# Optimization experiments

Measured on AMD Instinct MI355X. Metric: run time of the kernel, lower is better.

Reference implementation:

```python
import jax, jax.numpy as jnp
import numpy as np
import math

N_HEAD = 16
K_SPARSE = 64

def setup_inputs() -> dict:
    key = jax.random.key(0)
    ks = jax.random.split(key, 12)
    B, T, C = 1, 2048, 1024
    s = 0.02
    return {
        "x":   jax.random.normal(ks[0], (B, T, C), jnp.float32),
        "Wq":  jax.random.normal(ks[1], (C, C), jnp.float32) * s,
        "bq":  jax.random.normal(ks[2], (C,), jnp.float32) * s,
        "Wk":  jax.random.normal(ks[3], (C, C), jnp.float32) * s,
        "bk":  jax.random.normal(ks[4], (C,), jnp.float32) * s,
        "Wv":  jax.random.normal(ks[5], (C, C), jnp.float32) * s,
        "bv":  jax.random.normal(ks[6], (C,), jnp.float32) * s,
        "Wo":  jax.random.normal(ks[7], (C, C), jnp.float32) * s,
        "bo":  jax.random.normal(ks[8], (C,), jnp.float32) * s,
        "Wks": jax.random.normal(ks[9], (C,), jnp.float32) * s,
        "bks": jax.random.normal(ks[10], (), jnp.float32) * s,
    }

def reference(x, Wq, bq, Wk, bk, Wv, bv, Wo, bo, Wks, bks):
    B, T, C = x.shape
    nh = N_HEAD
    hs = C // nh
    k_val = min(K_SPARSE, T)

    # projections -> (B, nh, T, hs)   (torch Linear: x @ W.T + b)
    q = (x @ Wq.T + bq).reshape(B, T, nh, hs).transpose(0, 2, 1, 3)
    k = (x @ Wk.T + bk).reshape(B, T, nh, hs).transpose(0, 2, 1, 3)
    v = (x @ Wv.T + bv).reshape(B, T, nh, hs).transpose(0, 2, 1, 3)

    # key scorer: per-token scalar score (B, T)
    key_scores = x @ Wks + bks

    # causal masking of scores, then per-query top-k key selection
    pos = jnp.arange(T)
    causal = pos[None, :] <= pos[:, None]                      # (T, T), True where key<=query
    masked = jnp.where(causal[None], key_scores[:, None, :], -jnp.inf)  # (B, T, T)
    _, top_k_idx = jax.lax.top_k(masked, k_val)                # (B, T, k)
    top_k_idx = jnp.minimum(top_k_idx, pos[None, :, None])     # clamp to <= query pos

    # gather sparse keys/values: (B, nh, T, k, hs)
    bi = jnp.arange(B)[:, None, None, None]
    hi = jnp.arange(nh)[None, :, None, None]
    gi = top_k_idx[:, None, :, :]                              # (B, 1, T, k)
    sparse_k = k[bi, hi, gi]                                   # (B, nh, T, k, hs)
    sparse_v = v[bi, hi, gi]

    scale = 1.0 / math.sqrt(hs)
    logits = jnp.einsum('bhtd,bhtkd->bhtk', q, sparse_k) * scale
    probs = jax.nn.softmax(logits, axis=-1)
    out = jnp.einsum('bhtk,bhtkd->bhtd', probs, sparse_v)      # (B, nh, T, hs)
    out = out.transpose(0, 2, 1, 3).reshape(B, T, C)
    return out @ Wo.T + bo
```

## Files before the change

### kernel.cpp

```cpp
#include <hip/hip_runtime.h>
#include <hip/hip_bf16.h>
#include <cstdint>
#include <cstddef>

#define T_DIM 2048
#define C_DIM 1024
#define NH 16
#define HS 64
#define KSP 64

#define GBM 128
#define GBN 64
#define GBK 128
#define OBM 64
#define OBN 64

#define ATB 16
#define KLS 72
#define VTS 108
#define PLS 104
#define CNS 104

typedef short short8 __attribute__((ext_vector_type(8)));
typedef float f32x4 __attribute__((ext_vector_type(4)));
typedef _Float16 half8 __attribute__((ext_vector_type(8)));

__device__ __forceinline__ unsigned short f2bfu(float f) {
  unsigned u = __builtin_bit_cast(unsigned, f);
  unsigned r = (u + 0x7fffu + ((u >> 16) & 1u)) >> 16;
  return (unsigned short)r;
}
__device__ __forceinline__ unsigned short f2h(float f) {
  _Float16 h = (_Float16)f;
  return __builtin_bit_cast(unsigned short, h);
}

#define GLOAD_LDS16(gp, lp)                                                  \
  __builtin_amdgcn_global_load_lds(                                          \
      (const __attribute__((address_space(1))) void*)(gp),                   \
      (__attribute__((address_space(3))) void*)(lp), 16, 0, 0)

#define NSCORE (T_DIM / 4)
#define NCONV ((T_DIM * C_DIM + 4 * C_DIM * C_DIM) / 4 / 256)
__global__ __launch_bounds__(256) void convert_scores_kernel(
    const float* __restrict__ x, const float* __restrict__ Wq,
    const float* __restrict__ Wk, const float* __restrict__ Wv,
    const float* __restrict__ Wo, const float* __restrict__ Wks,
    const float* __restrict__ bks,
    unsigned short* __restrict__ xb, unsigned short* __restrict__ Wqb,
    unsigned short* __restrict__ Wkb, unsigned short* __restrict__ Wvb,
    unsigned short* __restrict__ Wob, float* __restrict__ scores) {
  if (blockIdx.x < NSCORE) {
    const int t = blockIdx.x * 4 + (threadIdx.x >> 6);
    const int lane = threadIdx.x & 63;
    const float* xrow = x + (size_t)t * C_DIM;
    float acc = 0.f;
    #pragma unroll 4
    for (int i = lane; i < C_DIM; i += 64)
      acc += xrow[i] * Wks[i];
    #pragma unroll
    for (int o = 32; o; o >>= 1) acc += __shfl_xor(acc, o);
    if (lane == 0) scores[t] = acc + bks[0];
    return;
  }
  const int i = (blockIdx.x - NSCORE) * 256 + threadIdx.x;
  const int NX4 = T_DIM * C_DIM / 4;
  const int NW4 = C_DIM * C_DIM / 4;
  const float* src;
  unsigned short* dst;
  int j = i;
  if (j < NX4) { src = x; dst = xb; }
  else {
    j -= NX4;
    int w = j / NW4;
    j -= w * NW4;
    src = (w == 0) ? Wq : (w == 1) ? Wk : (w == 2) ? Wv : Wo;
    dst = (w == 0) ? Wqb : (w == 1) ? Wkb : (w == 2) ? Wvb : Wob;
  }
  float4 f = reinterpret_cast<const float4*>(src)[j];
  ushort4 o;
  o.x = f2bfu(f.x); o.y = f2bfu(f.y); o.z = f2bfu(f.z); o.w = f2bfu(f.w);
  reinterpret_cast<ushort4*>(dst)[j] = o;
}

__device__ __forceinline__ void gemm_body_128x64(
    const unsigned short* __restrict__ A, const unsigned short* __restrict__ W,
    f32x4 acc[4][2], int bm, int bn, int tid,
    unsigned short* As, unsigned short* Ws) {
  const int w = tid >> 6, lane = tid & 63;
  const int quad = lane >> 4, r = lane & 15;
  const int wm = (w >> 1) * 64, wn = (w & 1) * 32;
  const int sub = lane >> 4;
  const int c = lane & 15;
  const unsigned short* Arow[8];
  const unsigned short* Wrow[4];
  #pragma unroll
  for (int i = 0; i < 8; ++i) {
    const int row = w * 32 + i * 4 + sub;
    Arow[i] = A + (size_t)(bm * GBM + row) * C_DIM + ((c ^ (row & 7)) * 8);
  }
  #pragma unroll
  for (int i = 0; i < 4; ++i) {
    const int row = w * 16 + i * 4 + sub;
    Wrow[i] = W + (size_t)(bn * GBN + row) * C_DIM + ((c ^ (row & 7)) * 8);
  }
  for (int kb = 0; kb < C_DIM; kb += GBK) {
    #pragma unroll
    for (int i = 0; i < 8; ++i)
      GLOAD_LDS16(Arow[i] + kb, &As[(w * 32 + i * 4) * GBK]);
    #pragma unroll
    for (int i = 0; i < 4; ++i)
      GLOAD_LDS16(Wrow[i] + kb, &Ws[(w * 16 + i * 4) * GBK]);
    __syncthreads();
    #pragma unroll
    for (int ks = 0; ks < 4; ++ks) {
      const int pc = ((ks * 4 + quad) ^ (r & 7)) * 8;
      short8 af[4], bfr[2];
      #pragma unroll
      for (int mi = 0; mi < 4; ++mi)
        af[mi] = *reinterpret_cast<const short8*>(&As[(wm + mi * 16 + r) * GBK + pc]);
      #pragma unroll
      for (int ni = 0; ni < 2; ++ni)
        bfr[ni] = *reinterpret_cast<const short8*>(&Ws[(wn + ni * 16 + r) * GBK + pc]);
      #pragma unroll
      for (int mi = 0; mi < 4; ++mi)
        #pragma unroll
        for (int ni = 0; ni < 2; ++ni)
          acc[mi][ni] = __builtin_amdgcn_mfma_f32_16x16x32_bf16(af[mi], bfr[ni], acc[mi][ni], 0, 0, 0);
    }
    __syncthreads();
  }
}

#define NRANK (T_DIM / 4)
__global__ __launch_bounds__(256) void gemm_qkv_rank_kernel(
    const unsigned short* __restrict__ A,
    const unsigned short* __restrict__ Wq, const unsigned short* __restrict__ Wk,
    const unsigned short* __restrict__ Wv,
    const float* __restrict__ bq, const float* __restrict__ bk,
    const float* __restrict__ bv,
    unsigned short* __restrict__ qo, unsigned short* __restrict__ ko,
    unsigned short* __restrict__ vo,
    const float* __restrict__ scores, int* __restrict__ sorted_idx) {
  __shared__ unsigned short lds[(GBM + GBN) * GBK];
  const int tid = threadIdx.x;
  if (blockIdx.x < NRANK) {
    float* ss = reinterpret_cast<float*>(lds);
    for (int j = tid; j < T_DIM; j += 256) ss[j] = scores[j];
    __syncthreads();
    const int w = tid >> 6, lane = tid & 63;
    const int i = blockIdx.x * 4 + w;
    const float si = ss[i];
    int rank = 0;
    #pragma unroll
    for (int step = 0; step < T_DIM / 64; ++step) {
      const int j = step * 64 + lane;
      const float sj = ss[j];
      rank += (int)((sj > si) || (sj == si && j < i));
    }
    #pragma unroll
    for (int o = 32; o; o >>= 1) rank += __shfl_xor(rank, o);
    if (lane == 0) sorted_idx[rank] = i;
    return;
  }
  const int bid = blockIdx.x - NRANK;
  const int per = (T_DIM / GBM) * (C_DIM / GBN);
  const int which = bid / per;
  const int rem = bid % per;
  const int bm = rem / (C_DIM / GBN);
  const int bn = rem % (C_DIM / GBN);
  const unsigned short* W = (which == 0) ? Wq : (which == 1) ? Wk : Wv;
  const float* bias = (which == 0) ? bq : (which == 1) ? bk : bv;
  unsigned short* out = (which == 0) ? qo : (which == 1) ? ko : vo;
  f32x4 acc[4][2] = {};
  gemm_body_128x64(A, W, acc, bm, bn, tid, lds, lds + GBM * GBK);
  const int w = tid >> 6, lane = tid & 63;
  const int quad = lane >> 4, r = lane & 15;
  const int wm = (w >> 1) * 64, wn = (w & 1) * 32;
  #pragma unroll
  for (int mi = 0; mi < 4; ++mi) {
    #pragma unroll
    for (int ni = 0; ni < 2; ++ni) {
      const int col = bn * GBN + wn + ni * 16 + r;
      const float bf = bias[col];
      #pragma unroll
      for (int i = 0; i < 4; ++i) {
        const int row = bm * GBM + wm + mi * 16 + quad * 4 + i;
        const float val = acc[mi][ni][i] + bf;
        out[(size_t)row * C_DIM + col] = f2h(val);
      }
    }
  }
}

__device__ __forceinline__ void gemm_body_64x64(
    const unsigned short* __restrict__ A, const unsigned short* __restrict__ W,
    f32x4 acc[2][2], int bm, int bn, int tid) {
  __shared__ unsigned short As[OBM * GBK];
  __shared__ unsigned short Ws[OBN * GBK];
  const int w = tid >> 6, lane = tid & 63;
  const int quad = lane >> 4, r = lane & 15;
  const int wm = (w >> 1) * 32, wn = (w & 1) * 32;
  const int sub = lane >> 4;
  const int c = lane & 15;
  const unsigned short* Arow[4];
  const unsigned short* Wrow[4];
  #pragma unroll
  for (int i = 0; i < 4; ++i) {
    const int row = w * 16 + i * 4 + sub;
    Arow[i] = A + (size_t)(bm * OBM + row) * C_DIM + ((c ^ (row & 7)) * 8);
    Wrow[i] = W + (size_t)(bn * OBN + row) * C_DIM + ((c ^ (row & 7)) * 8);
  }
  for (int kb = 0; kb < C_DIM; kb += GBK) {
    #pragma unroll
    for (int i = 0; i < 4; ++i)
      GLOAD_LDS16(Arow[i] + kb, &As[(w * 16 + i * 4) * GBK]);
    #pragma unroll
    for (int i = 0; i < 4; ++i)
      GLOAD_LDS16(Wrow[i] + kb, &Ws[(w * 16 + i * 4) * GBK]);
    __syncthreads();
    #pragma unroll
    for (int ks = 0; ks < 4; ++ks) {
      const int pc = ((ks * 4 + quad) ^ (r & 7)) * 8;
      short8 af[2], bfr[2];
      #pragma unroll
      for (int mi = 0; mi < 2; ++mi)
        af[mi] = *reinterpret_cast<const short8*>(&As[(wm + mi * 16 + r) * GBK + pc]);
      #pragma unroll
      for (int ni = 0; ni < 2; ++ni)
        bfr[ni] = *reinterpret_cast<const short8*>(&Ws[(wn + ni * 16 + r) * GBK + pc]);
      #pragma unroll
      for (int mi = 0; mi < 2; ++mi)
        #pragma unroll
        for (int ni = 0; ni < 2; ++ni)
          acc[mi][ni] = __builtin_amdgcn_mfma_f32_16x16x32_bf16(af[mi], bfr[ni], acc[mi][ni], 0, 0, 0);
    }
    __syncthreads();
  }
}

__global__ __launch_bounds__(256) void gemm_o_f32_kernel(
    const unsigned short* __restrict__ A, const unsigned short* __restrict__ W,
    const float* __restrict__ bias, float* __restrict__ out) {
  const int tid = threadIdx.x;
  const int bm = blockIdx.x / (C_DIM / OBN);
  const int bn = blockIdx.x % (C_DIM / OBN);
  f32x4 acc[2][2] = {};
  gemm_body_64x64(A, W, acc, bm, bn, tid);
  const int w = tid >> 6, lane = tid & 63;
  const int quad = lane >> 4, r = lane & 15;
  const int wm = (w >> 1) * 32, wn = (w & 1) * 32;
  #pragma unroll
  for (int mi = 0; mi < 2; ++mi) {
    #pragma unroll
    for (int ni = 0; ni < 2; ++ni) {
      const int col = bn * OBN + wn + ni * 16 + r;
      const float bf = bias[col];
      #pragma unroll
      for (int i = 0; i < 4; ++i) {
        const int row = bm * OBM + wm + mi * 16 + quad * 4 + i;
        out[(size_t)row * C_DIM + col] = acc[mi][ni][i] + bf;
      }
    }
  }
}

__global__ __launch_bounds__(256) void select_kernel(
    const int* __restrict__ sorted_idx, unsigned short* __restrict__ sel) {
  const int tid = threadIdx.x;
  const int w = tid >> 6, lane = tid & 63;
  const int t = blockIdx.x * 4 + w;
  unsigned short* dst = sel + (size_t)t * KSP;
  if (t <= 63) {
    dst[lane] = (unsigned short)((lane < t) ? lane : t);
    return;
  }
  const unsigned long long lt_mask = (1ull << lane) - 1ull;
  int count = 0;
  for (int c = 0; c < T_DIM / 64 && count < KSP; ++c) {
    int s = sorted_idx[c * 64 + lane];
    s = (s < 0) ? 0 : (s > T_DIM - 1 ? T_DIM - 1 : s);
    const bool ok = (s <= t);
    const unsigned long long mm = __ballot(ok);
    const int pos = count + __popcll(mm & lt_mask);
    if (ok && pos < KSP) dst[pos] = (unsigned short)s;
    count += __popcll(mm);
  }
}

__global__ __launch_bounds__(128) void attn_kernel(
    const unsigned short* __restrict__ q, const unsigned short* __restrict__ k,
    const unsigned short* __restrict__ v, const unsigned short* __restrict__ sel,
    unsigned short* __restrict__ attn_out) {
  __shared__ unsigned short Kl[2][80 * KLS];
  __shared__ unsigned short Vt[2][64 * VTS];
  __shared__ unsigned short Pl[2][16 * PLS];
  __shared__ unsigned int   cnt[16 * CNS];
  __shared__ short map_s[T_DIM];
  __shared__ short urows[80];
  const int tb = blockIdx.x >> 3;
  const int hg = blockIdx.x & 7;
  const int t0 = tb * ATB;
  const int tid = threadIdx.x;
  const int w = tid >> 6, lane = tid & 63;
  const int qd = lane >> 4;
  const int r = lane & 15;
  const int h = hg * 2 + w;

  uint4 qf[2];
  #pragma unroll
  for (int kc = 0; kc < 2; ++kc)
    qf[kc] = *reinterpret_cast<const uint4*>(
        q + (size_t)(t0 + r) * C_DIM + h * HS + kc * 32 + qd * 8);

  if (tid < KSP) {
    const int r0 = sel[(size_t)t0 * KSP + tid];
    map_s[r0] = (short)tid;
    urows[tid] = (short)r0;
  } else if (tid < 79) {
    const int row = t0 + 1 + (tid - KSP);
    map_s[row] = (short)tid;
    urows[tid] = (short)row;
  } else if (tid == 79) {
    urows[79] = (short)t0;
  }
  for (int i = tid; i < 16 * CNS; i += 128) cnt[i] = 0u;
  __syncthreads();

  {
    const int e8 = lane & 7;
    const int pr = lane >> 3;
    #pragma unroll
    for (int sb = 0; sb < 5; ++sb) {
      const int s0 = sb * 16 + pr * 2;
      const int row0 = urows[s0], row1 = urows[s0 + 1];
      const size_t g0 = (size_t)row0 * C_DIM + h * HS + e8 * 8;
      const size_t g1 = (size_t)row1 * C_DIM + h * HS + e8 * 8;
      const uint4 k0 = *reinterpret_cast<const uint4*>(k + g0);
      const uint4 k1 = *reinterpret_cast<const uint4*>(k + g1);
      const uint4 v0 = *reinterpret_cast<const uint4*>(v + g0);
      const uint4 v1 = *reinterpret_cast<const uint4*>(v + g1);
      *reinterpret_cast<uint4*>(&Kl[w][s0 * KLS + ((e8 ^ (s0 & 7)) * 8)]) = k0;
      *reinterpret_cast<uint4*>(&Kl[w][(s0 + 1) * KLS + ((e8 ^ ((s0 + 1) & 7)) * 8)]) = k1;
      const unsigned* v0w = reinterpret_cast<const unsigned*>(&v0);
      const unsigned* v1w = reinterpret_cast<const unsigned*>(&v1);
      #pragma unroll
      for (int dd = 0; dd < 8; ++dd) {
        const unsigned lo = (v0w[dd >> 1] >> ((dd & 1) * 16)) & 0xffffu;
        const unsigned hi = (v1w[dd >> 1] >> ((dd & 1) * 16)) & 0xffffu;
        *reinterpret_cast<unsigned*>(&Vt[w][(e8 * 8 + dd) * VTS + s0]) =
            lo | (hi << 16);
      }
    }
    #pragma unroll
    for (int z = 0; z < 4; ++z)
      *reinterpret_cast<unsigned long long*>(&Vt[w][lane * VTS + 80 + z * 4]) = 0ull;
    if (t0 < 64) {
      #pragma unroll
      for (int e = 0; e < 8; ++e) {
        const int idx = tid + e * 128;
        const int tl = idx >> 6;
        const int rr = sel[(size_t)(t0 + tl) * KSP + (idx & 63)];
        atomicAdd(&cnt[tl * CNS + map_s[rr]], 1u);
      }
    } else {
      #pragma unroll
      for (int e = 0; e < 8; ++e) {
        const int idx = tid + e * 128;
        const int tl = idx >> 6;
        const int rr = sel[(size_t)(t0 + tl) * KSP + (idx & 63)];
        cnt[tl * CNS + map_s[rr]] = 1u;
      }
    }
  }
  __syncthreads();

  f32x4 s5[5] = {};
  #pragma unroll
  for (int ut = 0; ut < 5; ++ut) {
    #pragma unroll
    for (int kc = 0; kc < 2; ++kc) {
      const uint4 kw = *reinterpret_cast<const uint4*>(
          &Kl[w][(ut * 16 + r) * KLS + (((kc * 4 + qd) ^ (r & 7)) * 8)]);
      s5[ut] = __builtin_amdgcn_mfma_f32_16x16x32_f16(
          __builtin_bit_cast(half8, kw), __builtin_bit_cast(half8, qf[kc]),
          s5[ut], 0, 0, 0);
    }
  }
  float mx = -3.0e38f;
  #pragma unroll
  for (int ut = 0; ut < 5; ++ut) {
    const uint4 c4 = *reinterpret_cast<const uint4*>(&cnt[r * CNS + ut * 16 + qd * 4]);
    const unsigned cc[4] = {c4.x, c4.y, c4.z, c4.w};
    #pragma unroll
    for (int i = 0; i < 4; ++i) {
      float lg = s5[ut][i] * 0.125f;
      lg = (cc[i] == 0u) ? -3.0e38f
         : (cc[i] == 1u) ? lg : (lg + __logf((float)cc[i]));
      s5[ut][i] = lg;
      mx = fmaxf(mx, lg);
    }
  }
  mx = fmaxf(mx, __shfl_xor(mx, 16));
  mx = fmaxf(mx, __shfl_xor(mx, 32));
  float sum = 0.f;
  #pragma unroll
  for (int ut = 0; ut < 5; ++ut)
    #pragma unroll
    for (int i = 0; i < 4; ++i) {
      const float e = __expf(s5[ut][i] - mx);
      s5[ut][i] = e;
      sum += e;
    }
  sum += __shfl_xor(sum, 16);
  sum += __shfl_xor(sum, 32);
  const float rs = 1.0f / sum;
  #pragma unroll
  for (int ut = 0; ut < 5; ++ut) {
    const unsigned w0 = (unsigned)f2h(s5[ut][0] * rs) |
                        ((unsigned)f2h(s5[ut][1] * rs) << 16);
    const unsigned w1 = (unsigned)f2h(s5[ut][2] * rs) |
                        ((unsigned)f2h(s5[ut][3] * rs) << 16);
    unsigned* p32 = reinterpret_cast<unsigned*>(&Pl[w][r * PLS + ut * 16 + qd * 4]);
    p32[0] = w0;
    p32[1] = w1;
  }
  *reinterpret_cast<unsigned long long*>(&Pl[w][r * PLS + 80 + qd * 4]) = 0ull;
  f32x4 o4[4] = {};
  #pragma unroll
  for (int c = 0; c < 3; ++c) {
    const uint4 pw = *reinterpret_cast<const uint4*>(&Pl[w][r * PLS + c * 32 + qd * 8]);
    #pragma unroll
    for (int mt = 0; mt < 4; ++mt) {
      const uint2 lo = *reinterpret_cast<const uint2*>(
          &Vt[w][(mt * 16 + r) * VTS + c * 32 + qd * 8]);
      const uint2 hi = *reinterpret_cast<const uint2*>(
          &Vt[w][(mt * 16 + r) * VTS + c * 32 + qd * 8 + 4]);
      const uint4 vw = {lo.x, lo.y, hi.x, hi.y};
      o4[mt] = __builtin_amdgcn_mfma_f32_16x16x32_f16(
          __builtin_bit_cast(half8, vw), __builtin_bit_cast(half8, pw),
          o4[mt], 0, 0, 0);
    }
  }
  #pragma unroll
  for (int mt = 0; mt < 4; ++mt) {
    ushort4 ov;
    ov.x = f2bfu(o4[mt][0]); ov.y = f2bfu(o4[mt][1]);
    ov.z = f2bfu(o4[mt][2]); ov.w = f2bfu(o4[mt][3]);
    *reinterpret_cast<ushort4*>(
        attn_out + (size_t)(t0 + r) * C_DIM + h * HS + mt * 16 + qd * 4) = ov;
  }
}

extern "C" void kernel_launch(void* const* d_in, const int* in_sizes, int n_in,
                              void* d_out, int out_size, void* d_ws, size_t ws_size,
                              hipStream_t stream) {
  const float* x   = (const float*)d_in[0];
  const float* Wq  = (const float*)d_in[1];
  const float* bq  = (const float*)d_in[2];
  const float* Wk  = (const float*)d_in[3];
  const float* bk  = (const float*)d_in[4];
  const float* Wv  = (const float*)d_in[5];
  const float* bv  = (const float*)d_in[6];
  const float* Wo  = (const float*)d_in[7];
  const float* bo  = (const float*)d_in[8];
  const float* Wks = (const float*)d_in[9];
  const float* bks = (const float*)d_in[10];
  float* out = (float*)d_out;

  char* ws = (char*)d_ws;
  size_t off = 0;
  float* scores = (float*)(ws + off); off += 8192;
  int*   sorted = (int*)(ws + off);   off += 8192;
  unsigned short* selb = (unsigned short*)(ws + off); off += (size_t)T_DIM * KSP * 2;
  unsigned short* xb  = (unsigned short*)(ws + off); off += (size_t)T_DIM * C_DIM * 2;
  unsigned short* Wqb = (unsigned short*)(ws + off); off += (size_t)C_DIM * C_DIM * 2;
  unsigned short* Wkb = (unsigned short*)(ws + off); off += (size_t)C_DIM * C_DIM * 2;
  unsigned short* Wvb = (unsigned short*)(ws + off); off += (size_t)C_DIM * C_DIM * 2;
  unsigned short* Wob = (unsigned short*)(ws + off); off += (size_t)C_DIM * C_DIM * 2;
  unsigned short* qb  = (unsigned short*)(ws + off); off += (size_t)T_DIM * C_DIM * 2;
  unsigned short* kb  = (unsigned short*)(ws + off); off += (size_t)T_DIM * C_DIM * 2;
  unsigned short* vb  = (unsigned short*)(ws + off); off += (size_t)T_DIM * C_DIM * 2;
  unsigned short* ab  = xb;

  convert_scores_kernel<<<NSCORE + NCONV, 256, 0, stream>>>(
      x, Wq, Wk, Wv, Wo, Wks, bks, xb, Wqb, Wkb, Wvb, Wob, scores);

  gemm_qkv_rank_kernel<<<NRANK + 3 * (T_DIM / GBM) * (C_DIM / GBN), 256, 0,
                         stream>>>(
      xb, Wqb, Wkb, Wvb, bq, bk, bv, qb, kb, vb, scores, sorted);

  select_kernel<<<T_DIM / 4, 256, 0, stream>>>(sorted, selb);

  attn_kernel<<<(T_DIM / ATB) * (NH / 2), 128, 0, stream>>>(qb, kb, vb, selb, ab);

  gemm_o_f32_kernel<<<(T_DIM / OBM) * (C_DIM / OBN), 256, 0, stream>>>(
      ab, Wob, bo, out);
}
```

Before: 149.9 us.

## Precompute per-tile row map and counts in prep kernel; enlarge output GEMM tile

```diff
diff --git a/kernel.cpp b/kernel.cpp
--- a/kernel.cpp
+++ b/kernel.cpp
@@ -12,14 +12,12 @@
 #define GBM 128
 #define GBN 64
 #define GBK 128
-#define OBM 64
-#define OBN 64
 
 #define ATB 16
-#define KLS 72
-#define VTS 108
-#define PLS 104
-#define CNS 104
+#define NTILE (T_DIM / ATB)
+#define KLS 64
+#define VTS 102
+#define PLS 96
 
 typedef short short8 __attribute__((ext_vector_type(8)));
 typedef float f32x4 __attribute__((ext_vector_type(4)));
@@ -193,111 +191,111 @@
   }
 }
 
-__device__ __forceinline__ void gemm_body_64x64(
-    const unsigned short* __restrict__ A, const unsigned short* __restrict__ W,
-    f32x4 acc[2][2], int bm, int bn, int tid) {
-  __shared__ unsigned short As[OBM * GBK];
-  __shared__ unsigned short Ws[OBN * GBK];
-  const int w = tid >> 6, lane = tid & 63;
-  const int quad = lane >> 4, r = lane & 15;
-  const int wm = (w >> 1) * 32, wn = (w & 1) * 32;
-  const int sub = lane >> 4;
-  const int c = lane & 15;
-  const unsigned short* Arow[4];
-  const unsigned short* Wrow[4];
-  #pragma unroll
-  for (int i = 0; i < 4; ++i) {
-    const int row = w * 16 + i * 4 + sub;
-    Arow[i] = A + (size_t)(bm * OBM + row) * C_DIM + ((c ^ (row & 7)) * 8);
-    Wrow[i] = W + (size_t)(bn * OBN + row) * C_DIM + ((c ^ (row & 7)) * 8);
-  }
-  for (int kb = 0; kb < C_DIM; kb += GBK) {
-    #pragma unroll
-    for (int i = 0; i < 4; ++i)
-      GLOAD_LDS16(Arow[i] + kb, &As[(w * 16 + i * 4) * GBK]);
-    #pragma unroll
-    for (int i = 0; i < 4; ++i)
-      GLOAD_LDS16(Wrow[i] + kb, &Ws[(w * 16 + i * 4) * GBK]);
-    __syncthreads();
-    #pragma unroll
-    for (int ks = 0; ks < 4; ++ks) {
-      const int pc = ((ks * 4 + quad) ^ (r & 7)) * 8;
-      short8 af[2], bfr[2];
-      #pragma unroll
-      for (int mi = 0; mi < 2; ++mi)
-        af[mi] = *reinterpret_cast<const short8*>(&As[(wm + mi * 16 + r) * GBK + pc]);
-      #pragma unroll
-      for (int ni = 0; ni < 2; ++ni)
-        bfr[ni] = *reinterpret_cast<const short8*>(&Ws[(wn + ni * 16 + r) * GBK + pc]);
-      #pragma unroll
-      for (int mi = 0; mi < 2; ++mi)
-        #pragma unroll
-        for (int ni = 0; ni < 2; ++ni)
-          acc[mi][ni] = __builtin_amdgcn_mfma_f32_16x16x32_bf16(af[mi], bfr[ni], acc[mi][ni], 0, 0, 0);
-    }
-    __syncthreads();
-  }
-}
-
 __global__ __launch_bounds__(256) void gemm_o_f32_kernel(
     const unsigned short* __restrict__ A, const unsigned short* __restrict__ W,
     const float* __restrict__ bias, float* __restrict__ out) {
+  __shared__ unsigned short lds[(GBM + GBN) * GBK];
   const int tid = threadIdx.x;
-  const int bm = blockIdx.x / (C_DIM / OBN);
-  const int bn = blockIdx.x % (C_DIM / OBN);
-  f32x4 acc[2][2] = {};
-  gemm_body_64x64(A, W, acc, bm, bn, tid);
+  const int bm = blockIdx.x / (C_DIM / GBN);
+  const int bn = blockIdx.x % (C_DIM / GBN);
+  f32x4 acc[4][2] = {};
+  gemm_body_128x64(A, W, acc, bm, bn, tid, lds, lds + GBM * GBK);
   const int w = tid >> 6, lane = tid & 63;
   const int quad = lane >> 4, r = lane & 15;
-  const int wm = (w >> 1) * 32, wn = (w & 1) * 32;
-  #pragma unroll
-  for (int mi = 0; mi < 2; ++mi) {
+  const int wm = (w >> 1) * 64, wn = (w & 1) * 32;
+  #pragma unroll
+  for (int mi = 0; mi < 4; ++mi) {
     #pragma unroll
     for (int ni = 0; ni < 2; ++ni) {
-      const int col = bn * OBN + wn + ni * 16 + r;
+      const int col = bn * GBN + wn + ni * 16 + r;
       const float bf = bias[col];
       #pragma unroll
       for (int i = 0; i < 4; ++i) {
-        const int row = bm * OBM + wm + mi * 16 + quad * 4 + i;
+        const int row = bm * GBM + wm + mi * 16 + quad * 4 + i;
         out[(size_t)row * C_DIM + col] = acc[mi][ni][i] + bf;
       }
     }
   }
 }
 
-__global__ __launch_bounds__(256) void select_kernel(
-    const int* __restrict__ sorted_idx, unsigned short* __restrict__ sel) {
+__global__ __launch_bounds__(256) void prep_kernel(
+    const int* __restrict__ sorted_idx,
+    unsigned short* __restrict__ urows_g,
+    unsigned char* __restrict__ cnt_g) {
+  __shared__ unsigned short rows_tab[ATB][KSP];
+  __shared__ unsigned char map_s[T_DIM];
+  __shared__ unsigned int cnt_l[16 * 80];
+  const int tile = blockIdx.x;
+  const int t0 = tile * ATB;
   const int tid = threadIdx.x;
   const int w = tid >> 6, lane = tid & 63;
-  const int t = blockIdx.x * 4 + w;
-  unsigned short* dst = sel + (size_t)t * KSP;
-  if (t <= 63) {
-    dst[lane] = (unsigned short)((lane < t) ? lane : t);
-    return;
-  }
-  const unsigned long long lt_mask = (1ull << lane) - 1ull;
-  int count = 0;
-  for (int c = 0; c < T_DIM / 64 && count < KSP; ++c) {
-    int s = sorted_idx[c * 64 + lane];
-    s = (s < 0) ? 0 : (s > T_DIM - 1 ? T_DIM - 1 : s);
-    const bool ok = (s <= t);
-    const unsigned long long mm = __ballot(ok);
-    const int pos = count + __popcll(mm & lt_mask);
-    if (ok && pos < KSP) dst[pos] = (unsigned short)s;
-    count += __popcll(mm);
-  }
+  if (t0 <= 48) {
+    #pragma unroll
+    for (int li = 0; li < 4; ++li) {
+      const int t = t0 + w * 4 + li;
+      rows_tab[w * 4 + li][lane] = (unsigned short)((lane < t) ? lane : t);
+    }
+  } else {
+    const unsigned long long lt_mask = (1ull << lane) - 1ull;
+    const int tw = t0 + w * 4;
+    int c4[4] = {0, 0, 0, 0};
+    for (int c = 0; c < T_DIM / 64 && c4[0] < KSP; ++c) {
+      int s = sorted_idx[c * 64 + lane];
+      s = (s < 0) ? 0 : (s > T_DIM - 1 ? T_DIM - 1 : s);
+      #pragma unroll
+      for (int li = 0; li < 4; ++li) {
+        const bool ok = (s <= tw + li);
+        const unsigned long long mm = __ballot(ok);
+        const int pos = c4[li] + __popcll(mm & lt_mask);
+        if (ok && pos < KSP) rows_tab[w * 4 + li][pos] = (unsigned short)s;
+        c4[li] += __popcll(mm);
+      }
+    }
+  }
+  for (int i = tid; i < 16 * 80; i += 256) cnt_l[i] = 0u;
+  __syncthreads();
+  if (tid < KSP) {
+    const int r0 = rows_tab[0][tid];
+    map_s[r0] = (unsigned char)tid;
+    urows_g[(size_t)tile * 80 + tid] = (unsigned short)r0;
+  } else if (tid < 79) {
+    const int row = t0 + 1 + (tid - KSP);
+    map_s[row] = (unsigned char)tid;
+    urows_g[(size_t)tile * 80 + tid] = (unsigned short)row;
+  } else if (tid == 79) {
+    urows_g[(size_t)tile * 80 + 79] = (unsigned short)t0;
+  }
+  __syncthreads();
+  if (t0 < 64) {
+    #pragma unroll
+    for (int e = 0; e < 4; ++e) {
+      const int idx = tid + e * 256;
+      atomicAdd(&cnt_l[(idx >> 6) * 80 + map_s[rows_tab[idx >> 6][idx & 63]]], 1u);
+    }
+  } else {
+    #pragma unroll
+    for (int e = 0; e < 4; ++e) {
+      const int idx = tid + e * 256;
+      cnt_l[(idx >> 6) * 80 + map_s[rows_tab[idx >> 6][idx & 63]]] = 1u;
+    }
+  }
+  __syncthreads();
+  unsigned* cg = reinterpret_cast<unsigned*>(cnt_g + (size_t)tile * 1280);
+  for (int i = tid; i < 320; i += 256)
+    cg[i] = (cnt_l[4 * i] & 0xffu) | ((cnt_l[4 * i + 1] & 0xffu) << 8) |
+            ((cnt_l[4 * i + 2] & 0xffu) << 16) | ((cnt_l[4 * i + 3] & 0xffu) << 24);
 }
 
 __global__ __launch_bounds__(128) void attn_kernel(
     const unsigned short* __restrict__ q, const unsigned short* __restrict__ k,
-    const unsigned short* __restrict__ v, const unsigned short* __restrict__ sel,
+    const unsigned short* __restrict__ v,
+    const unsigned short* __restrict__ urows_g,
+    const unsigned char* __restrict__ cnt_g,
     unsigned short* __restrict__ attn_out) {
   __shared__ unsigned short Kl[2][80 * KLS];
   __shared__ unsigned short Vt[2][64 * VTS];
   __shared__ unsigned short Pl[2][16 * PLS];
-  __shared__ unsigned int   cnt[16 * CNS];
-  __shared__ short map_s[T_DIM];
-  __shared__ short urows[80];
+  __shared__ unsigned short urows[80];
   const int tb = blockIdx.x >> 3;
   const int hg = blockIdx.x & 7;
   const int t0 = tb * ATB;
@@ -306,25 +304,12 @@
   const int qd = lane >> 4;
   const int r = lane & 15;
   const int h = hg * 2 + w;
-
+  if (tid < 80) urows[tid] = urows_g[(size_t)tb * 80 + tid];
   uint4 qf[2];
   #pragma unroll
   for (int kc = 0; kc < 2; ++kc)
     qf[kc] = *reinterpret_cast<const uint4*>(
         q + (size_t)(t0 + r) * C_DIM + h * HS + kc * 32 + qd * 8);
-
-  if (tid < KSP) {
-    const int r0 = sel[(size_t)t0 * KSP + tid];
-    map_s[r0] = (short)tid;
-    urows[tid] = (short)r0;
-  } else if (tid < 79) {
-    const int row = t0 + 1 + (tid - KSP);
-    map_s[row] = (short)tid;
-    urows[tid] = (short)row;
-  } else if (tid == 79) {
-    urows[79] = (short)t0;
-  }
-  for (int i = tid; i < 16 * CNS; i += 128) cnt[i] = 0u;
   __syncthreads();
 
   {
@@ -353,25 +338,8 @@
       }
     }
     #pragma unroll
-    for (int z = 0; z < 4; ++z)
-      *reinterpret_cast<unsigned long long*>(&Vt[w][lane * VTS + 80 + z * 4]) = 0ull;
-    if (t0 < 64) {
-      #pragma unroll
-      for (int e = 0; e < 8; ++e) {
-        const int idx = tid + e * 128;
-        const int tl = idx >> 6;
-        const int rr = sel[(size_t)(t0 + tl) * KSP + (idx & 63)];
-        atomicAdd(&cnt[tl * CNS + map_s[rr]], 1u);
-      }
-    } else {
-      #pragma unroll
-      for (int e = 0; e < 8; ++e) {
-        const int idx = tid + e * 128;
-        const int tl = idx >> 6;
-        const int rr = sel[(size_t)(t0 + tl) * KSP + (idx & 63)];
-        cnt[tl * CNS + map_s[rr]] = 1u;
-      }
-    }
+    for (int z = 0; z < 8; ++z)
+      *reinterpret_cast<unsigned*>(&Vt[w][lane * VTS + 80 + z * 2]) = 0u;
   }
   __syncthreads();
 
@@ -387,16 +355,17 @@
           s5[ut], 0, 0, 0);
     }
   }
+  const unsigned char* cb = cnt_g + (size_t)tb * 1280 + r * 80;
   float mx = -3.0e38f;
   #pragma unroll
   for (int ut = 0; ut < 5; ++ut) {
-    const uint4 c4 = *reinterpret_cast<const uint4*>(&cnt[r * CNS + ut * 16 + qd * 4]);
-    const unsigned cc[4] = {c4.x, c4.y, c4.z, c4.w};
+    const unsigned c4 = *reinterpret_cast<const unsigned*>(cb + ut * 16 + qd * 4);
     #pragma unroll
     for (int i = 0; i < 4; ++i) {
+      const unsigned cc = (c4 >> (8 * i)) & 0xffu;
       float lg = s5[ut][i] * 0.125f;
-      lg = (cc[i] == 0u) ? -3.0e38f
-         : (cc[i] == 1u) ? lg : (lg + __logf((float)cc[i]));
+      lg = (cc == 0u) ? -3.0e38f
+         : (cc == 1u) ? lg : (lg + __logf((float)cc));
       s5[ut][i] = lg;
       mx = fmaxf(mx, lg);
     }
@@ -432,11 +401,12 @@
     const uint4 pw = *reinterpret_cast<const uint4*>(&Pl[w][r * PLS + c * 32 + qd * 8]);
     #pragma unroll
     for (int mt = 0; mt < 4; ++mt) {
-      const uint2 lo = *reinterpret_cast<const uint2*>(
-          &Vt[w][(mt * 16 + r) * VTS + c * 32 + qd * 8]);
-      const uint2 hi = *reinterpret_cast<const uint2*>(
-          &Vt[w][(mt * 16 + r) * VTS + c * 32 + qd * 8 + 4]);
-      const uint4 vw = {lo.x, lo.y, hi.x, hi.y};
+      const unsigned short* vb_ = &Vt[w][(mt * 16 + r) * VTS + c * 32 + qd * 8];
+      uint4 vw;
+      vw.x = *reinterpret_cast<const unsigned*>(vb_);
+      vw.y = *reinterpret_cast<const unsigned*>(vb_ + 2);
+      vw.z = *reinterpret_cast<const unsigned*>(vb_ + 4);
+      vw.w = *reinterpret_cast<const unsigned*>(vb_ + 6);
       o4[mt] = __builtin_amdgcn_mfma_f32_16x16x32_f16(
           __builtin_bit_cast(half8, vw), __builtin_bit_cast(half8, pw),
           o4[mt], 0, 0, 0);
@@ -472,7 +442,9 @@
   size_t off = 0;
   float* scores = (float*)(ws + off); off += 8192;
   int*   sorted = (int*)(ws + off);   off += 8192;
-  unsigned short* selb = (unsigned short*)(ws + off); off += (size_t)T_DIM * KSP * 2;
+  unsigned short* urowsb = (unsigned short*)(ws + off); off += (size_t)NTILE * 80 * 2;
+  unsigned char*  cntb   = (unsigned char*)(ws + off);  off += (size_t)NTILE * 1280;
+  off = (off + 255) & ~(size_t)255;
   unsigned short* xb  = (unsigned short*)(ws + off); off += (size_t)T_DIM * C_DIM * 2;
   unsigned short* Wqb = (unsigned short*)(ws + off); off += (size_t)C_DIM * C_DIM * 2;
   unsigned short* Wkb = (unsigned short*)(ws + off); off += (size_t)C_DIM * C_DIM * 2;
@@ -490,10 +462,10 @@
                          stream>>>(
       xb, Wqb, Wkb, Wvb, bq, bk, bv, qb, kb, vb, scores, sorted);
 
-  select_kernel<<<T_DIM / 4, 256, 0, stream>>>(sorted, selb);
-
-  attn_kernel<<<(T_DIM / ATB) * (NH / 2), 128, 0, stream>>>(qb, kb, vb, selb, ab);
-
-  gemm_o_f32_kernel<<<(T_DIM / OBM) * (C_DIM / OBN), 256, 0, stream>>>(
+  prep_kernel<<<NTILE, 256, 0, stream>>>(sorted, urowsb, cntb);
+
+  attn_kernel<<<NTILE * (NH / 2), 128, 0, stream>>>(qb, kb, vb, urowsb, cntb, ab);
+
+  gemm_o_f32_kernel<<<(T_DIM / GBM) * (C_DIM / GBN), 256, 0, stream>>>(
       ab, Wob, bo, out);
 }
```

New measurement: 156.4 us. 4.4% more time.

## Shrink attention LDS footprint with aliased arena and byte-sized count maps

Applied to the files above, without the earlier changes.

```diff
diff --git a/kernel.cpp b/kernel.cpp
--- a/kernel.cpp
+++ b/kernel.cpp
@@ -16,10 +16,9 @@
 #define OBN 64
 
 #define ATB 16
-#define KLS 72
-#define VTS 108
-#define PLS 104
-#define CNS 104
+#define KLS 64
+#define VTS 102
+#define PLS 96
 
 typedef short short8 __attribute__((ext_vector_type(8)));
 typedef float f32x4 __attribute__((ext_vector_type(4)));
@@ -292,12 +291,13 @@
     const unsigned short* __restrict__ q, const unsigned short* __restrict__ k,
     const unsigned short* __restrict__ v, const unsigned short* __restrict__ sel,
     unsigned short* __restrict__ attn_out) {
-  __shared__ unsigned short Kl[2][80 * KLS];
-  __shared__ unsigned short Vt[2][64 * VTS];
-  __shared__ unsigned short Pl[2][16 * PLS];
-  __shared__ unsigned int   cnt[16 * CNS];
-  __shared__ short map_s[T_DIM];
-  __shared__ short urows[80];
+  __shared__ __align__(16) unsigned char arena[52896];
+  unsigned short* KlB = reinterpret_cast<unsigned short*>(arena);
+  unsigned short* VtB = reinterpret_cast<unsigned short*>(arena + 20480);
+  unsigned short* PlB = reinterpret_cast<unsigned short*>(arena + 46592);
+  unsigned char* map8 = arena + 46592;
+  unsigned char* cnt8 = arena + 46592 + 2048;
+  unsigned short* urows = reinterpret_cast<unsigned short*>(arena + 52736);
   const int tb = blockIdx.x >> 3;
   const int hg = blockIdx.x & 7;
   const int t0 = tb * ATB;
@@ -306,6 +306,9 @@
   const int qd = lane >> 4;
   const int r = lane & 15;
   const int h = hg * 2 + w;
+  unsigned short* Klw = KlB + w * 80 * KLS;
+  unsigned short* Vtw = VtB + w * 64 * VTS;
+  unsigned short* Plw = PlB + w * 16 * PLS;
 
   uint4 qf[2];
   #pragma unroll
@@ -315,16 +318,19 @@
 
   if (tid < KSP) {
     const int r0 = sel[(size_t)t0 * KSP + tid];
-    map_s[r0] = (short)tid;
-    urows[tid] = (short)r0;
+    urows[tid] = (unsigned short)r0;
+    if (t0 >= 64) map8[r0] = (unsigned char)tid;
   } else if (tid < 79) {
     const int row = t0 + 1 + (tid - KSP);
-    map_s[row] = (short)tid;
-    urows[tid] = (short)row;
+    urows[tid] = (unsigned short)row;
+    if (t0 >= 64) map8[row] = (unsigned char)tid;
   } else if (tid == 79) {
-    urows[79] = (short)t0;
-  }
-  for (int i = tid; i < 16 * CNS; i += 128) cnt[i] = 0u;
+    urows[79] = (unsigned short)t0;
+  }
+  if (t0 >= 64) {
+    for (int i = tid; i < 320; i += 128)
+      reinterpret_cast<unsigned*>(cnt8)[i] = 0u;
+  }
   __syncthreads();
 
   {
@@ -340,36 +346,43 @@
       const uint4 k1 = *reinterpret_cast<const uint4*>(k + g1);
       const uint4 v0 = *reinterpret_cast<const uint4*>(v + g0);
       const uint4 v1 = *reinterpret_cast<const uint4*>(v + g1);
-      *reinterpret_cast<uint4*>(&Kl[w][s0 * KLS + ((e8 ^ (s0 & 7)) * 8)]) = k0;
-      *reinterpret_cast<uint4*>(&Kl[w][(s0 + 1) * KLS + ((e8 ^ ((s0 + 1) & 7)) * 8)]) = k1;
+      *reinterpret_cast<uint4*>(&Klw[s0 * KLS + ((e8 ^ (s0 & 7)) * 8)]) = k0;
+      *reinterpret_cast<uint4*>(&Klw[(s0 + 1) * KLS + ((e8 ^ ((s0 + 1) & 7)) * 8)]) = k1;
       const unsigned* v0w = reinterpret_cast<const unsigned*>(&v0);
       const unsigned* v1w = reinterpret_cast<const unsigned*>(&v1);
       #pragma unroll
       for (int dd = 0; dd < 8; ++dd) {
         const unsigned lo = (v0w[dd >> 1] >> ((dd & 1) * 16)) & 0xffffu;
         const unsigned hi = (v1w[dd >> 1] >> ((dd & 1) * 16)) & 0xffffu;
-        *reinterpret_cast<unsigned*>(&Vt[w][(e8 * 8 + dd) * VTS + s0]) =
+        *reinterpret_cast<unsigned*>(&Vtw[(e8 * 8 + dd) * VTS + s0]) =
             lo | (hi << 16);
       }
     }
     #pragma unroll
-    for (int z = 0; z < 4; ++z)
-      *reinterpret_cast<unsigned long long*>(&Vt[w][lane * VTS + 80 + z * 4]) = 0ull;
-    if (t0 < 64) {
+    for (int z = 0; z < 8; ++z)
+      *reinterpret_cast<unsigned*>(&Vtw[lane * VTS + 80 + z * 2]) = 0u;
+    if (t0 >= 64) {
       #pragma unroll
       for (int e = 0; e < 8; ++e) {
         const int idx = tid + e * 128;
         const int tl = idx >> 6;
         const int rr = sel[(size_t)(t0 + tl) * KSP + (idx & 63)];
-        atomicAdd(&cnt[tl * CNS + map_s[rr]], 1u);
+        cnt8[tl * 80 + map8[rr]] = 1;
       }
-    } else {
-      #pragma unroll
-      for (int e = 0; e < 8; ++e) {
-        const int idx = tid + e * 128;
-        const int tl = idx >> 6;
-        const int rr = sel[(size_t)(t0 + tl) * KSP + (idx & 63)];
-        cnt[tl * CNS + map_s[rr]] = 1u;
+    } else if (tid < 80) {
+      const int s = tid;
+      #pragma unroll
+      for (int tl = 0; tl < ATB; ++tl) {
+        const int t = t0 + tl;
+        int c;
+        if (s < t0)        c = 1;
+        else if (s == t0)  c = (tl == 0) ? (64 - t) : 1;
+        else if (s < 64)   c = 0;
+        else if (s < 79) {
+          const int row = t0 + 1 + (s - 64);
+          c = (row < t) ? 1 : ((row == t) ? (64 - t) : 0);
+        } else c = 0;
+        cnt8[tl * 80 + s] = (unsigned char)c;
       }
     }
   }
@@ -381,7 +394,7 @@
     #pragma unroll
     for (int kc = 0; kc < 2; ++kc) {
       const uint4 kw = *reinterpret_cast<const uint4*>(
-          &Kl[w][(ut * 16 + r) * KLS + (((kc * 4 + qd) ^ (r & 7)) * 8)]);
+          &Klw[(ut * 16 + r) * KLS + (((kc * 4 + qd) ^ (r & 7)) * 8)]);
       s5[ut] = __builtin_amdgcn_mfma_f32_16x16x32_f16(
           __builtin_bit_cast(half8, kw), __builtin_bit_cast(half8, qf[kc]),
           s5[ut], 0, 0, 0);
@@ -390,13 +403,14 @@
   float mx = -3.0e38f;
   #pragma unroll
   for (int ut = 0; ut < 5; ++ut) {
-    const uint4 c4 = *reinterpret_cast<const uint4*>(&cnt[r * CNS + ut * 16 + qd * 4]);
-    const unsigned cc[4] = {c4.x, c4.y, c4.z, c4.w};
+    const unsigned c4 =
+        *reinterpret_cast<const unsigned*>(cnt8 + r * 80 + ut * 16 + qd * 4);
     #pragma unroll
     for (int i = 0; i < 4; ++i) {
+      const unsigned cc = (c4 >> (8 * i)) & 0xffu;
       float lg = s5[ut][i] * 0.125f;
-      lg = (cc[i] == 0u) ? -3.0e38f
-         : (cc[i] == 1u) ? lg : (lg + __logf((float)cc[i]));
+      lg = (cc == 0u) ? -3.0e38f
+         : (cc == 1u) ? lg : (lg + __logf((float)cc));
       s5[ut][i] = lg;
       mx = fmaxf(mx, lg);
     }
@@ -415,28 +429,30 @@
   sum += __shfl_xor(sum, 16);
   sum += __shfl_xor(sum, 32);
   const float rs = 1.0f / sum;
+  __syncthreads();
   #pragma unroll
   for (int ut = 0; ut < 5; ++ut) {
     const unsigned w0 = (unsigned)f2h(s5[ut][0] * rs) |
                         ((unsigned)f2h(s5[ut][1] * rs) << 16);
     const unsigned w1 = (unsigned)f2h(s5[ut][2] * rs) |
                         ((unsigned)f2h(s5[ut][3] * rs) << 16);
-    unsigned* p32 = reinterpret_cast<unsigned*>(&Pl[w][r * PLS + ut * 16 + qd * 4]);
+    unsigned* p32 = reinterpret_cast<unsigned*>(&Plw[r * PLS + ut * 16 + qd * 4]);
     p32[0] = w0;
     p32[1] = w1;
   }
-  *reinterpret_cast<unsigned long long*>(&Pl[w][r * PLS + 80 + qd * 4]) = 0ull;
+  *reinterpret_cast<unsigned long long*>(&Plw[r * PLS + 80 + qd * 4]) = 0ull;
   f32x4 o4[4] = {};
   #pragma unroll
   for (int c = 0; c < 3; ++c) {
-    const uint4 pw = *reinterpret_cast<const uint4*>(&Pl[w][r * PLS + c * 32 + qd * 8]);
+    const uint4 pw = *reinterpret_cast<const uint4*>(&Plw[r * PLS + c * 32 + qd * 8]);
     #pragma unroll
     for (int mt = 0; mt < 4; ++mt) {
-      const uint2 lo = *reinterpret_cast<const uint2*>(
-          &Vt[w][(mt * 16 + r) * VTS + c * 32 + qd * 8]);
-      const uint2 hi = *reinterpret_cast<const uint2*>(
-          &Vt[w][(mt * 16 + r) * VTS + c * 32 + qd * 8 + 4]);
-      const uint4 vw = {lo.x, lo.y, hi.x, hi.y};
+      const unsigned short* vb_ = &Vtw[(mt * 16 + r) * VTS + c * 32 + qd * 8];
+      uint4 vw;
+      vw.x = *reinterpret_cast<const unsigned*>(vb_);
+      vw.y = *reinterpret_cast<const unsigned*>(vb_ + 2);
+      vw.z = *reinterpret_cast<const unsigned*>(vb_ + 4);
+      vw.w = *reinterpret_cast<const unsigned*>(vb_ + 6);
       o4[mt] = __builtin_amdgcn_mfma_f32_16x16x32_f16(
           __builtin_bit_cast(half8, vw), __builtin_bit_cast(half8, pw),
           o4[mt], 0, 0, 0);
```

New measurement: 146.5 us. 1.02x faster.
